# Performance work log

Hardware: AMD Instinct MI355X
Metric: run time of the kernel (lower is better)

Reference implementation:

```python
import jax, jax.numpy as jnp
import numpy as np

EMB = 2048
HEADS = 16


def setup_inputs() -> dict:
    key = jax.random.key(0)
    k_x, k_wqkv, k_bqkv, k_wo, k_bo = jax.random.split(key, 5)
    B, S, E = 2, 2048, EMB
    x = jax.random.normal(k_x, (B, S, E), dtype=jnp.float32)
    # nn.Linear weights stored as (in, out) for x @ W + b convention
    W_qkv = jax.random.normal(k_wqkv, (E, 3 * E), dtype=jnp.float32) * 0.02
    b_qkv = jax.random.normal(k_bqkv, (3 * E,), dtype=jnp.float32) * 0.02
    W_out = jax.random.normal(k_wo, (E, E), dtype=jnp.float32) * 0.02
    b_out = jax.random.normal(k_bo, (E,), dtype=jnp.float32) * 0.02
    return {"x": x, "W_qkv": W_qkv, "b_qkv": b_qkv, "W_out": W_out, "b_out": b_out}


def reference(x, W_qkv, b_qkv, W_out, b_out):
    B, S, E = x.shape
    H = HEADS
    dh = E // H
    # QKV projection: (B,S,3E)
    qkv = x @ W_qkv + b_qkv
    # Faithful to torch: reshape (B,S,H,3*dh) THEN split -> interleaved per-head q/k/v
    qkv = qkv.reshape(B, S, H, 3 * dh).transpose(0, 2, 1, 3)  # (B,H,S,3*dh)
    q, k, v = jnp.split(qkv, 3, axis=-1)  # each (B,H,S,dh)
    q = q / jnp.asarray(dh, q.dtype) ** 0.5
    scores = jnp.einsum('bhqd,bhkd->bhqk', q, k)  # (B,H,S,S)
    weights = jax.nn.softmax(scores, axis=-1)
    attn = jnp.einsum('bhqk,bhkd->bhqd', weights, v)  # (B,H,S,dh)
    attn = attn.transpose(0, 2, 1, 3).reshape(B, S, E)
    return attn @ W_out + b_out
```

## Files before the change

kernel.cpp:

```cpp
#include <hip/hip_runtime.h>
#include <type_traits>
#include <utility>

#define DI __device__ __forceinline__

typedef unsigned short u16;
typedef float f32x4 __attribute__((ext_vector_type(4)));
typedef float f32x16 __attribute__((ext_vector_type(16)));
typedef short s16x8 __attribute__((ext_vector_type(8)));
typedef __bf16 bf16x8 __attribute__((ext_vector_type(8)));

template <typename V, typename = void>
struct mfma_ok : std::false_type {};
template <typename V>
struct mfma_ok<V, std::void_t<decltype(__builtin_amdgcn_mfma_f32_16x16x32_bf16(
    std::declval<V>(), std::declval<V>(), std::declval<f32x4>(), 0, 0, 0))>>
    : std::true_type {};
using frag_t = std::conditional_t<mfma_ok<bf16x8>::value, bf16x8, s16x8>;

union U128 {
  int4 i;
  frag_t f;
  u16 s[8];
};

DI f32x4 mfma16(const U128& a, const U128& b, f32x4 c) {
  return __builtin_amdgcn_mfma_f32_16x16x32_bf16(a.f, b.f, c, 0, 0, 0);
}
DI f32x16 mfma32(const U128& a, const U128& b, f32x16 c) {
  return __builtin_amdgcn_mfma_f32_32x32x16_bf16(a.f, b.f, c, 0, 0, 0);
}

DI u16 f2b(float x) {
  union { float f; unsigned u; } v; v.f = x;
  unsigned r = v.u + 0x7FFFu + ((v.u >> 16) & 1u);
  return (u16)(r >> 16);
}

DI unsigned pk2bf(float a, float b) {
  unsigned short ua = __builtin_bit_cast(unsigned short, (__bf16)a);
  unsigned short ub = __builtin_bit_cast(unsigned short, (__bf16)b);
  return (unsigned)ua | ((unsigned)ub << 16);
}

#if __has_builtin(__builtin_amdgcn_exp2f)
#define EXP2F __builtin_amdgcn_exp2f
#else
#define EXP2F exp2f
#endif

DI void plswap(unsigned& lo, unsigned& hi) {
  asm("v_permlane32_swap_b32 %0, %1" : "+v"(lo), "+v"(hi));
}

typedef __attribute__((address_space(1))) void gas_t;
typedef __attribute__((address_space(3))) void las_t;
DI void gll16(const void* g, void* l) {
  __builtin_amdgcn_global_load_lds((gas_t*)g, (las_t*)l, 16, 0, 0);
}

#define QSCALE 0.12751791437603762f

DI void transpose_tile(const float* __restrict__ in, u16* __restrict__ out,
                       int R, int C, int bx, int by, int t, u16 (*Tb)[68]) {
  long r0 = (long)by * 64, c0 = (long)bx * 64;
  int cq = (t & 15) * 4, rr = t >> 4;
#pragma unroll
  for (int it = 0; it < 4; ++it) {
    int r = rr + it * 16;
    float4 v = *(const float4*)(in + (r0 + r) * C + c0 + cq);
    Tb[r][cq + 0] = f2b(v.x); Tb[r][cq + 1] = f2b(v.y);
    Tb[r][cq + 2] = f2b(v.z); Tb[r][cq + 3] = f2b(v.w);
  }
  __syncthreads();
#pragma unroll
  for (int it = 0; it < 2; ++it) {
    int ci = it * 256 + t;
    int cc = ci >> 3, ch = ci & 7, rb = ch * 8;
    unsigned p0 = Tb[rb + 0][cc] | ((unsigned)Tb[rb + 1][cc] << 16);
    unsigned p1 = Tb[rb + 2][cc] | ((unsigned)Tb[rb + 3][cc] << 16);
    unsigned p2 = Tb[rb + 4][cc] | ((unsigned)Tb[rb + 5][cc] << 16);
    unsigned p3 = Tb[rb + 6][cc] | ((unsigned)Tb[rb + 7][cc] << 16);
    *(int4*)(out + (c0 + cc) * R + r0 + rb) = make_int4(p0, p1, p2, p3);
  }
}

__global__ __launch_bounds__(256) void k_pre(const float* __restrict__ x,
                                             u16* __restrict__ xb,
                                             const float* __restrict__ Wqkv,
                                             u16* __restrict__ wqkvt) {
  __shared__ __attribute__((aligned(16))) u16 Tb[64][68];
  int bid = blockIdx.x, t = threadIdx.x;
  if (bid < 8192) {
    int i = bid * 256 + t;
    float4 v = ((const float4*)x)[i];
    ushort4 o;
    o.x = f2b(v.x); o.y = f2b(v.y); o.z = f2b(v.z); o.w = f2b(v.w);
    ((ushort4*)xb)[i] = o;
    return;
  }
  int idx = bid - 8192;
  transpose_tile(Wqkv, wqkvt, 2048, 6144, idx % 96, idx / 96, t, Tb);
}

template <int MODE>
__global__ __launch_bounds__(256, 4) void k_gemm_bt(const u16* __restrict__ A,
                                                    const u16* __restrict__ Bt,
                                                    const float* __restrict__ bias,
                                                    void* __restrict__ Cout,
                                                    u16* __restrict__ qb,
                                                    u16* __restrict__ kbv,
                                                    u16* __restrict__ vt,
                                                    int n_off,
                                                    int M, int N, int K) {
  __shared__ __attribute__((aligned(16))) u16 SM[16384];
  u16* As = SM;
  u16* Bs = SM + 8192;
  int t = threadIdx.x;
  int lane = t & 63, w = t >> 6, quad = lane >> 4, l15 = lane & 15;
  long m0 = (long)blockIdx.y * 128, n0 = n_off + (long)blockIdx.x * 128;
  int wr = (w >> 1) * 64, wc = (w & 1) * 64;
  int sw = l15 & 7;
  f32x4 acc[4][4] = {};
  for (int k0 = 0; k0 < K; k0 += 64) {
    __syncthreads();
#pragma unroll
    for (int it = 0; it < 4; ++it) {
      int ci = it * 256 + t;
      int row = ci >> 3, cl = (ci & 7) ^ (row & 7);
      gll16(A + (m0 + row) * K + k0 + cl * 8, As + ci * 8);
      gll16(Bt + (n0 + row) * K + k0 + cl * 8, Bs + ci * 8);
    }
    __syncthreads();
#pragma unroll
    for (int kk = 0; kk < 2; ++kk) {
      U128 a[4], b[4];
#pragma unroll
      for (int i = 0; i < 4; ++i)
        a[i].i = *(const int4*)(As + (wr + i * 16 + l15) * 64 + (((kk * 4 + quad) ^ sw) << 3));
#pragma unroll
      for (int j = 0; j < 4; ++j)
        b[j].i = *(const int4*)(Bs + (wc + j * 16 + l15) * 64 + (((kk * 4 + quad) ^ sw) << 3));
#pragma unroll
      for (int i = 0; i < 4; ++i)
#pragma unroll
        for (int j = 0; j < 4; ++j)
          acc[i][j] = mfma16(a[i], b[j], acc[i][j]);
    }
  }
  float bj[4];
#pragma unroll
  for (int j = 0; j < 4; ++j) bj[j] = bias[n0 + wc + j * 16 + l15];

  int hidx = (int)(n0 / 384);
  int rsel = (int)(n0 - hidx * 384) >> 7;

  if (MODE == 1 && rsel == 2) {
    __syncthreads();
#pragma unroll
    for (int i = 0; i < 4; ++i)
#pragma unroll
      for (int rr2 = 0; rr2 < 4; ++rr2) {
        int m = wr + i * 16 + quad * 4 + rr2;
#pragma unroll
        for (int j = 0; j < 4; ++j) {
          int dd = wc + j * 16 + l15;
          SM[dd * 128 + (m ^ ((dd & 15) << 3))] = f2b(acc[i][j][rr2] + bj[j]);
        }
      }
    __syncthreads();
    int bidx = (int)(m0 >> 11);
    int stile = (int)((m0 & 2047) >> 7);
    u16* vtile = vt + (long)(bidx * 16 + hidx) * 262144 + stile * 16384;
#pragma unroll
    for (int it = 0; it < 8; ++it) {
      int ci = it * 256 + t;
      int d = ci >> 4, sb = (ci & 15) * 8;
      *(int4*)(vtile + d * 128 + sb) =
          *(const int4*)(SM + d * 128 + (sb ^ ((d & 15) << 3)));
    }
    return;
  }

  u16* route = (MODE == 1) ? (rsel == 0 ? qb : kbv) : nullptr;

#pragma unroll
  for (int i = 0; i < 4; ++i) {
#pragma unroll
    for (int rr2 = 0; rr2 < 4; ++rr2) {
      long row = m0 + wr + i * 16 + quad * 4 + rr2;
#pragma unroll
      for (int j = 0; j < 4; ++j) {
        float v = acc[i][j][rr2] + bj[j];
        if (MODE == 1) {
          if (rsel == 0) v *= QSCALE;
          int bidx = (int)(row >> 11), s = (int)(row & 2047);
          long obase = ((long)(bidx * 16 + hidx) * 2048 + s) * 128;
          int dh = wc + j * 16 + l15;
          unsigned pb = f2b(v);
          unsigned other = __shfl_xor(pb, 1);
          if (!(l15 & 1))
            ((unsigned*)route)[(obase + dh) >> 1] = pb | (other << 16);
        } else {
          long col = n0 + wc + j * 16 + l15;
          unsigned bits = __float_as_uint(v);
          unsigned other = __shfl_xor(bits, 1);
          if (!(l15 & 1)) {
            uint2 pr; pr.x = bits; pr.y = other;
            *(uint2*)((float*)Cout + row * N + col) = pr;
          }
        }
      }
    }
  }
}

__global__ __launch_bounds__(512, 2) void k_flash(const u16* __restrict__ qb,
                                                  const u16* __restrict__ kb,
                                                  const u16* __restrict__ vt,
                                                  u16* __restrict__ attn,
                                                  const float* __restrict__ Wout,
                                                  u16* __restrict__ woutt) {
  __shared__ __attribute__((aligned(16))) u16 Ks[2][128 * 128];
  __shared__ __attribute__((aligned(16))) u16 Vts[2][128 * 128];
  if (blockIdx.y >= 32) {
    int half = threadIdx.x >> 8, tt = threadIdx.x & 255;
    u16 (*Tb)[68] = (u16(*)[68])(&Ks[0][0] + half * 64 * 68);
    int ub = ((blockIdx.y - 32) * 8 + blockIdx.x) * 4 + half * 2;
#pragma unroll
    for (int rep = 0; rep < 2; ++rep) {
      int u = ub + rep;
      transpose_tile(Wout, woutt, 2048, 2048, u & 31, u >> 5, tt, Tb);
      __syncthreads();
    }
    return;
  }
  int t = threadIdx.x;
  int lane = t & 63, w = t >> 6, l31 = lane & 31, h = lane >> 5;
  int d0 = blockIdx.y * 8 + blockIdx.x;
  int bh = (d0 & 7) + ((d0 >> 6) << 3);
  int jq = (d0 >> 3) & 7;
  int q0 = jq * 256 + w * 32;
  int b = bh >> 4, hd = bh & 15;

  const u16* qbase = qb + ((long)bh * 2048 + q0 + l31) * 128;
  U128 qf[8];
#pragma unroll
  for (int dht = 0; dht < 8; ++dht)
    qf[dht].i = *(const int4*)(qbase + dht * 16 + h * 8);
  __syncthreads();

  f32x16 O[4] = {};
  float ls0 = 0.f, ls1 = 0.f, ls2 = 0.f, ls3 = 0.f;
  const u16* kbh = kb + (long)bh * 2048 * 128;
  long vbase = (long)bh * 262144;

  unsigned kinv = ((unsigned)l31 << 7) ^ (unsigned)(((l31 & 7) << 3) ^ (h << 3));

  auto stage = [&](int buf, int k0) {
#pragma unroll
    for (int it = 0; it < 4; ++it) {
      int ci = it * 512 + t;
      int key = ci >> 4, cp = ci & 15, cl = cp ^ (key & 7);
      gll16(kbh + (long)(k0 + key) * 128 + cl * 8, &Ks[buf][0] + ci * 8);
    }
#pragma unroll
    for (int it = 0; it < 4; ++it) {
      int ci = it * 512 + t;
      int d = ci >> 4, cp = ci & 15, cl = cp ^ (d & 7);
      gll16(vt + vbase + ((long)(k0 >> 7) << 14) + d * 128 + cl * 8,
            &Vts[buf][0] + ci * 8);
    }
  };

  stage(0, 0);
  int cur = 0;
  for (int k0 = 0; k0 < 2048; k0 += 128) {
    if (k0 + 128 < 2048) {
      stage(cur ^ 1, k0 + 128);
      asm volatile("s_waitcnt vmcnt(8)" ::: "memory");
    } else {
      asm volatile("s_waitcnt vmcnt(0)" ::: "memory");
    }
    __builtin_amdgcn_s_barrier();
    asm volatile("" ::: "memory");
    const u16* KbT = &Ks[cur][0];
    const u16* VbT = &Vts[cur][0];

    f32x16 St0 = {}, St1 = {}, St2 = {}, St3 = {};
    __builtin_amdgcn_s_setprio(1);
#pragma unroll
    for (int dht = 0; dht < 8; ++dht) {
      unsigned ka = kinv ^ (unsigned)(dht << 4);
      U128 k0f, k1f, k2f, k3f;
      k0f.i = *(const int4*)(KbT + ka);
      k1f.i = *(const int4*)(KbT + ka + 4096);
      k2f.i = *(const int4*)(KbT + ka + 8192);
      k3f.i = *(const int4*)(KbT + ka + 12288);
      St0 = mfma32(k0f, qf[dht], St0);
      St1 = mfma32(k1f, qf[dht], St1);
      St2 = mfma32(k2f, qf[dht], St2);
      St3 = mfma32(k3f, qf[dht], St3);
    }
    __builtin_amdgcn_s_setprio(0);

    auto pv = [&](int kt, const U128& pfk) {
#pragma unroll
      for (int dht = 0; dht < 4; ++dht) {
        U128 vf;
        vf.i = *(const int4*)(VbT + dht * 4096 + (kinv ^ (unsigned)(kt << 4)));
        O[dht] = mfma32(vf, pfk, O[dht]);
      }
    };
    auto mkpf = [&](const float* p) {
      unsigned w0 = pk2bf(p[0], p[1]);
      unsigned w1 = pk2bf(p[2], p[3]);
      unsigned w2 = pk2bf(p[4], p[5]);
      unsigned w3 = pk2bf(p[6], p[7]);
      plswap(w0, w2);
      plswap(w1, w3);
      U128 r; r.i = make_int4(w0, w1, w2, w3);
      return r;
    };
#define SM8(St, p, off)                                        \
    {                                                          \
      p[off + 0] = EXP2F(St[off + 0]); ls0 += p[off + 0];      \
      p[off + 1] = EXP2F(St[off + 1]); ls1 += p[off + 1];      \
      p[off + 2] = EXP2F(St[off + 2]); ls2 += p[off + 2];      \
      p[off + 3] = EXP2F(St[off + 3]); ls3 += p[off + 3];      \
      p[off + 4] = EXP2F(St[off + 4]); ls0 += p[off + 4];      \
      p[off + 5] = EXP2F(St[off + 5]); ls1 += p[off + 5];      \
      p[off + 6] = EXP2F(St[off + 6]); ls2 += p[off + 6];      \
      p[off + 7] = EXP2F(St[off + 7]); ls3 += p[off + 7];      \
    }

    float p0[16], p1[16], p2[16], p3[16];
    SM8(St0, p0, 0) SM8(St0, p0, 8)
    U128 pf0a = mkpf(&p0[0]), pf0b = mkpf(&p0[8]);
    pv(0, pf0a);
    SM8(St1, p1, 0)
    pv(1, pf0b);
    SM8(St1, p1, 8)
    U128 pf1a = mkpf(&p1[0]), pf1b = mkpf(&p1[8]);
    pv(2, pf1a);
    SM8(St2, p2, 0)
    pv(3, pf1b);
    SM8(St2, p2, 8)
    U128 pf2a = mkpf(&p2[0]), pf2b = mkpf(&p2[8]);
    pv(4, pf2a);
    SM8(St3, p3, 0)
    pv(5, pf2b);
    SM8(St3, p3, 8)
    U128 pf3a = mkpf(&p3[0]), pf3b = mkpf(&p3[8]);
    __builtin_amdgcn_s_setprio(1);
    pv(6, pf3a);
    pv(7, pf3b);
    __builtin_amdgcn_s_setprio(0);
#undef SM8

    asm volatile("" ::: "memory");
    __builtin_amdgcn_s_barrier();
    cur ^= 1;
  }

  float lsum = (ls0 + ls1) + (ls2 + ls3);
  float ltot = lsum + __shfl_xor(lsum, 32);
  float inv = 1.f / ltot;
  long orow = (long)b * 2048 + q0 + l31;
  u16* ob = attn + orow * 2048 + hd * 128;
#pragma unroll
  for (int dht = 0; dht < 4; ++dht)
#pragma unroll
    for (int g = 0; g < 4; ++g) {
      int dh = dht * 32 + g * 8 + h * 4;
      float v0 = O[dht][4 * g + 0] * inv, v1 = O[dht][4 * g + 1] * inv;
      float v2 = O[dht][4 * g + 2] * inv, v3 = O[dht][4 * g + 3] * inv;
      uint2 pkd;
      pkd.x = pk2bf(v0, v1);
      pkd.y = pk2bf(v2, v3);
      *(uint2*)(ob + dh) = pkd;
    }
}

extern "C" void kernel_launch(void* const* d_in, const int* in_sizes, int n_in,
                              void* d_out, int out_size, void* d_ws, size_t ws_size,
                              hipStream_t stream) {
  const float* x    = (const float*)d_in[0];
  const float* Wqkv = (const float*)d_in[1];
  const float* bqkv = (const float*)d_in[2];
  const float* Wout = (const float*)d_in[3];
  const float* bout = (const float*)d_in[4];
  float* out = (float*)d_out;
  char* ws = (char*)d_ws;

  if (ws_size < 75497472u) return;

  u16* xb    = (u16*)d_out;
  u16* wqkvt = (u16*)(ws);
  u16* qbuf  = (u16*)(ws + 25165824);
  u16* kbuf  = (u16*)(ws + 41943040);
  u16* vtb   = (u16*)(ws + 58720256);
  u16* woutt = (u16*)(ws);
  u16* attnb = (u16*)(ws + 8388608);

  k_pre<<<11264, 256, 0, stream>>>(x, xb, Wqkv, wqkvt);
  k_gemm_bt<1><<<dim3(48, 32), 256, 0, stream>>>(xb, wqkvt, bqkv, nullptr,
                                                 qbuf, kbuf, vtb, 0, 4096, 6144, 2048);
  k_flash<<<dim3(8, 64), 512, 0, stream>>>(qbuf, kbuf, vtb, attnb, Wout, woutt);
  k_gemm_bt<0><<<dim3(16, 32), 256, 0, stream>>>(attnb, woutt, bout, out,
                                                 nullptr, nullptr, nullptr, 0, 4096, 2048, 2048);
}
```

Measured before the change: 359.5 us.

## Add 256x256-tile QKV GEMM kernel with 4-stage pipeline for first two-thirds of N

Adds a new 512-thread QKV projection GEMM kernel with 256x256 output tiles, a 4-deep async global-to-LDS pipeline and swizzled LDS. It fuses bias, Q scaling and routing of Q/K rows plus the V transpose through shared memory. It covers the first 4096 output columns over a 16x16 grid, and the old 128x128 kernel handles the remaining 2048 columns via n_off. The larger tiles raise arithmetic intensity per LDS byte but use 128KB of LDS per block, which lowers occupancy, and the split means two launches.

```diff
diff --git a/kernel.cpp b/kernel.cpp
--- a/kernel.cpp
+++ b/kernel.cpp
@@ -101,6 +101,135 @@
   }
   int idx = bid - 8192;
   transpose_tile(Wqkv, wqkvt, 2048, 6144, idx % 96, idx / 96, t, Tb);
+}
+
+__global__ __launch_bounds__(512, 2) void k_gemm8r(const u16* __restrict__ A,
+                                                   const u16* __restrict__ Bt,
+                                                   const float* __restrict__ bias,
+                                                   u16* __restrict__ qb,
+                                                   u16* __restrict__ kbv,
+                                                   u16* __restrict__ vt,
+                                                   int M, int N, int K) {
+  __shared__ __attribute__((aligned(16))) u16 SH[65536];
+  int t = threadIdx.x;
+  int lane = t & 63, w = t >> 6, quad = lane >> 4, l15 = lane & 15;
+  int wm = w >> 2, wn = w & 3;
+  long m0 = (long)blockIdx.y * 256, n0 = (long)blockIdx.x * 256;
+  int sa = (l15 ^ (l15 >> 2)) & 3;
+  f32x4 acc[8][4] = {};
+
+  auto stage = [&](int j) {
+    u16* Ab = SH + (j & 3) * 16384;
+    u16* Bb = Ab + 8192;
+    long k0 = (long)j << 5;
+#pragma unroll
+    for (int it = 0; it < 2; ++it) {
+      int ci = it * 512 + t;
+      int row = ci >> 2, cp = ci & 3;
+      int cl = cp ^ ((row ^ (row >> 2)) & 3);
+      gll16(A + (m0 + row) * K + k0 + cl * 8, Ab + ci * 8);
+    }
+#pragma unroll
+    for (int it = 0; it < 2; ++it) {
+      int ci = it * 512 + t;
+      int row = ci >> 2, cp = ci & 3;
+      int cl = cp ^ ((row ^ (row >> 2)) & 3);
+      gll16(Bt + (n0 + row) * K + k0 + cl * 8, Bb + ci * 8);
+    }
+  };
+
+  int nt = K >> 5;
+  stage(0); stage(1); stage(2);
+  asm volatile("s_waitcnt vmcnt(8)" ::: "memory");
+  __builtin_amdgcn_s_barrier();
+  asm volatile("" ::: "memory");
+
+  for (int k = 0; k < nt; ++k) {
+    if (k + 3 < nt) stage(k + 3);
+    const u16* Ab = SH + (k & 3) * 16384;
+    const u16* Bb = Ab + 8192;
+    U128 a[8], b[4];
+#pragma unroll
+    for (int i = 0; i < 8; ++i)
+      a[i].i = *(const int4*)(Ab + (wm * 128 + i * 16 + l15) * 32 + ((quad ^ sa) << 3));
+#pragma unroll
+    for (int j = 0; j < 4; ++j)
+      b[j].i = *(const int4*)(Bb + (wn * 64 + j * 16 + l15) * 32 + ((quad ^ sa) << 3));
+    __builtin_amdgcn_s_setprio(1);
+#pragma unroll
+    for (int i = 0; i < 8; ++i)
+#pragma unroll
+      for (int j = 0; j < 4; ++j)
+        acc[i][j] = mfma16(a[i], b[j], acc[i][j]);
+    __builtin_amdgcn_s_setprio(0);
+    asm volatile("" ::: "memory");
+    if (k + 3 < nt)      asm volatile("s_waitcnt vmcnt(8)" ::: "memory");
+    else if (k + 2 < nt) asm volatile("s_waitcnt vmcnt(4)" ::: "memory");
+    else                 asm volatile("s_waitcnt vmcnt(0)" ::: "memory");
+    __builtin_amdgcn_s_barrier();
+    asm volatile("" ::: "memory");
+  }
+
+  float bj[4];
+#pragma unroll
+  for (int j = 0; j < 4; ++j) bj[j] = bias[n0 + wn * 64 + j * 16 + l15];
+
+  int g0 = (int)(n0 >> 7);
+  int vhalf = (g0 % 3 == 2) ? 0 : (((g0 + 1) % 3 == 2) ? 1 : -1);
+  int myhalf = wn >> 1;
+  int grp = g0 + myhalf;
+  int hidx = grp / 3, rsel = grp - hidx * 3;
+
+  if (myhalf == vhalf) {
+#pragma unroll
+    for (int i = 0; i < 8; ++i)
+#pragma unroll
+      for (int rr2 = 0; rr2 < 4; rr2 += 2)
+#pragma unroll
+        for (int j = 0; j < 4; ++j) {
+          int s = wm * 128 + i * 16 + quad * 4 + rr2;
+          int dd = (wn & 1) * 64 + j * 16 + l15;
+          unsigned pk = f2b(acc[i][j][rr2] + bj[j]) |
+                        ((unsigned)f2b(acc[i][j][rr2 + 1] + bj[j]) << 16);
+          *(unsigned*)(SH + dd * 256 + (s ^ ((dd & 15) << 3))) = pk;
+        }
+  } else {
+    u16* route = (rsel == 0) ? qb : kbv;
+#pragma unroll
+    for (int i = 0; i < 8; ++i)
+#pragma unroll
+      for (int rr2 = 0; rr2 < 4; ++rr2) {
+        long row = m0 + wm * 128 + i * 16 + quad * 4 + rr2;
+#pragma unroll
+        for (int j = 0; j < 4; ++j) {
+          float v = acc[i][j][rr2] + bj[j];
+          if (rsel == 0) v *= QSCALE;
+          int bidx = (int)(row >> 11), s = (int)(row & 2047);
+          long obase = ((long)(bidx * 16 + hidx) * 2048 + s) * 128;
+          int dh = (wn & 1) * 64 + j * 16 + l15;
+          unsigned pb = f2b(v);
+          unsigned other = __shfl_xor(pb, 1);
+          if (!(l15 & 1))
+            ((unsigned*)route)[(obase + dh) >> 1] = pb | (other << 16);
+        }
+      }
+  }
+  __builtin_amdgcn_s_barrier();
+  asm volatile("" ::: "memory");
+  if (myhalf == vhalf) {
+    int bidx = (int)(m0 >> 11);
+    int st0 = (int)((m0 & 2047) >> 7);
+    int vw = (wm << 1) | (wn & 1);
+    int tv = vw * 64 + lane;
+    u16* vb2 = vt + (long)(bidx * 16 + hidx) * 262144;
+#pragma unroll
+    for (int it = 0; it < 16; ++it) {
+      int ci = it * 256 + tv;
+      int d = ci >> 5, s8 = (ci & 31) * 8;
+      int4 v = *(const int4*)(SH + d * 256 + (s8 ^ ((d & 15) << 3)));
+      *(int4*)(vb2 + (long)(st0 + (s8 >> 7)) * 16384 + d * 128 + (s8 & 127)) = v;
+    }
+  }
 }
 
 template <int MODE>
@@ -404,8 +533,10 @@
   u16* attnb = (u16*)(ws + 8388608);
 
   k_pre<<<11264, 256, 0, stream>>>(x, xb, Wqkv, wqkvt);
-  k_gemm_bt<1><<<dim3(48, 32), 256, 0, stream>>>(xb, wqkvt, bqkv, nullptr,
-                                                 qbuf, kbuf, vtb, 0, 4096, 6144, 2048);
+  k_gemm8r<<<dim3(16, 16), 512, 0, stream>>>(xb, wqkvt, bqkv,
+                                             qbuf, kbuf, vtb, 4096, 4096, 2048);
+  k_gemm_bt<1><<<dim3(16, 32), 256, 0, stream>>>(xb, wqkvt, bqkv, nullptr,
+                                                 qbuf, kbuf, vtb, 4096, 4096, 6144, 2048);
   k_flash<<<dim3(8, 64), 512, 0, stream>>>(qbuf, kbuf, vtb, attnb, Wout, woutt);
   k_gemm_bt<0><<<dim3(16, 32), 256, 0, stream>>>(attnb, woutt, bout, out,
                                                  nullptr, nullptr, nullptr, 0, 4096, 2048, 2048);
```

New measurement: 390.6 us. 8.6% more time.
